# Performance work log

Measured on AMD Instinct MI355X. Metric: run time of the kernel, lower is better.

## Reference

```python
import jax, jax.numpy as jnp
import numpy as np

N = 50000   # nodes
E = 800000  # edges
IN = 128    # input_channels
HID = 256   # hidden_channels
G = 64      # graphs
R = 3       # num_relations
META = 38
EPS = 1e-5


def _glorot(key, shape):
    fan_in, fan_out = shape[-2], shape[-1]
    lim = np.sqrt(6.0 / (fan_in + fan_out)).astype(np.float32)
    return jax.random.uniform(key, shape, jnp.float32, -lim, lim)


def setup_inputs() -> dict:
    key = jax.random.key(0)
    ks = iter(jax.random.split(key, 40))
    inp = {}
    inp["x"] = jax.random.normal(next(ks), (N, IN), jnp.float32)
    inp["edge_attr"] = jax.random.normal(next(ks), (E, 1), jnp.float32)  # unused by module
    inp["edge_index"] = jax.random.randint(next(ks), (2, E), 0, N)
    inp["edge_type"] = jax.random.randint(next(ks), (E,), 0, R)
    inp["MetaData"] = jax.random.normal(next(ks), (G, META), jnp.float32)
    inp["batch"] = jnp.sort(jax.random.randint(next(ks), (N,), 0, G))
    dims = [(IN, 100), (100, HID), (HID, HID), (HID, HID)]
    for l, (din, dout) in enumerate(dims):
        inp[f"W{l}"] = _glorot(next(ks), (R, din, dout))      # per-relation weights
        inp[f"R{l}"] = _glorot(next(ks), (din, dout))          # root weight
        inp[f"b{l}"] = jnp.zeros((dout,), jnp.float32)         # conv bias
        inp[f"g{l}"] = jnp.ones((dout,), jnp.float32)          # BN gamma
        inp[f"bb{l}"] = jnp.zeros((dout,), jnp.float32)        # BN beta
    inp["lin1_w"] = _glorot(next(ks), (HID + META, 100))
    inp["lin1_b"] = jnp.zeros((100,), jnp.float32)
    inp["lin2_w"] = _glorot(next(ks), (100, 1))
    inp["lin2_b"] = jnp.zeros((1,), jnp.float32)
    return inp


def reference(x, edge_attr, edge_index, edge_type, MetaData, batch,
              W0, R0, b0, g0, bb0, W1, R1, b1, g1, bb1,
              W2, R2, b2, g2, bb2, W3, R3, b3, g3, bb3,
              lin1_w, lin1_b, lin2_w, lin2_b):
    src, dst = edge_index[0], edge_index[1]
    seg = edge_type * N + dst  # combined (relation, dst) segment id
    ones_e = jnp.ones((E,), x.dtype)
    cnt = jax.ops.segment_sum(ones_e, seg, num_segments=R * N).reshape(R, N, 1)
    cnt = jnp.maximum(cnt, 1.0)

    def conv(h, W, Rw, b):
        # per-relation transform then gather-scatter mean aggregation (PyG RGCNConv, aggr='mean')
        H = jnp.einsum('ni,rio->rno', h, W)          # [R,N,out]
        msg = H[edge_type, src]                       # [E,out]
        agg = jax.ops.segment_sum(msg, seg, num_segments=R * N)
        agg = agg.reshape(R, N, -1) / cnt
        return agg.sum(0) + h @ Rw + b

    def bn(h, g, bb):  # training-mode BatchNorm1d over nodes
        mu = h.mean(0)
        var = h.var(0)
        return (h - mu) * jax.lax.rsqrt(var + EPS) * g + bb

    for W, Rw, b, g, bb in [(W0, R0, b0, g0, bb0), (W1, R1, b1, g1, bb1),
                            (W2, R2, b2, g2, bb2), (W3, R3, b3, g3, bb3)]:
        x = bn(conv(x, W, Rw, b), g, bb)

    # global_mean_pool
    sums = jax.ops.segment_sum(x, batch, num_segments=G)
    cnts = jax.ops.segment_sum(jnp.ones((N, 1), x.dtype), batch, num_segments=G)
    xg = sums / jnp.maximum(cnts, 1.0)

    h = jnp.concatenate([xg, MetaData], axis=1) @ lin1_w + lin1_b
    # dropout p=0.5 is identity in eval mode
    return h @ lin2_w + lin2_b
```

## Files before the change

### kernel.cpp

```cpp
#include <hip/hip_runtime.h>
#include <hip/hip_bf16.h>

#define NN 50000
#define EE 800000
#define GG 64
#define RR 3
#define METAD 38
#define NSEG (RR*NN)
#define EPSV 1e-5f

typedef __bf16 bf_t;
typedef __attribute__((ext_vector_type(8))) __bf16 bf16x8;
typedef __attribute__((ext_vector_type(4))) __bf16 bf16x4;
typedef __attribute__((ext_vector_type(2))) __bf16 bf16x2;
typedef __attribute__((ext_vector_type(4))) float f32x4;
typedef __attribute__((address_space(1))) void gas_t;
typedef __attribute__((address_space(3))) void las_t;

__device__ __forceinline__ float loadf(const void* p, size_t i, int flag){
  return flag ? ((const float*)p)[i] : (float)(((const bf_t*)p)[i]);
}

__global__ __launch_bounds__(256) void detect_kernel(const void* __restrict__ xraw,
                                                     int* __restrict__ flag){
  __shared__ int found;
  if (threadIdx.x == 0) found = 0;
  __syncthreads();
  const unsigned short* u = (const unsigned short*)xraw;
  for (int i = threadIdx.x; i < 65536; i += 256){
    int e = (u[i] >> 7) & 0xFF;
    if (e >= 0xF0) found = 1;
  }
  __syncthreads();
  if (threadIdx.x == 0) *flag = found;
}

struct CvtJobs {
  const void* src[17];
  float* dst[17];
  int n[17];
};

__global__ __launch_bounds__(256) void cvt_many(CvtJobs j, const int* __restrict__ flag){
  int job = blockIdx.y;
  int i = blockIdx.x*256 + threadIdx.x;
  if (i < j.n[job]) j.dst[job][i] = loadf(j.src[job], i, *flag);
}

__global__ __launch_bounds__(256) void pack_w(const void* __restrict__ W,
                                              const void* __restrict__ R,
                                              bf_t* __restrict__ out,
                                              int D, int O, int dplog,
                                              const int* __restrict__ flag){
  int id = blockIdx.x*256 + threadIdx.x;
  int DP4 = 1 << (dplog + 2);
  int o = id >> (dplog + 2);
  int k = id & (DP4 - 1);
  int r = k >> dplog;
  int i = k & ((1 << dplog) - 1);
  float v = 0.f;
  int fl = *flag;
  if (i < D && o < O){
    if (r < 3) v = loadf(W, ((size_t)r*D + i)*O + o, fl);
    else       v = loadf(R, (size_t)i*O + o, fl);
  }
  out[(size_t)o*DP4 + k] = (bf_t)v;
}

__global__ __launch_bounds__(256) void counti_kernel(const int* __restrict__ ei,
                                                     const int* __restrict__ et,
                                                     int* __restrict__ cnt){
  int e = blockIdx.x*256 + threadIdx.x;
  if (e < EE) atomicAdd(&cnt[et[e]*NN + ei[EE + e]], 1);
}

__global__ __launch_bounds__(256) void rcnt_kernel(const int* __restrict__ cnt,
                                                   float* __restrict__ rcnt){
  int i = blockIdx.x*256 + threadIdx.x;
  if (i < NSEG) rcnt[i] = 1.0f / (float)max(cnt[i], 1);
}

__global__ __launch_bounds__(256) void scan1_kernel(const int* __restrict__ cnt,
                                                    int* __restrict__ segoff,
                                                    int* __restrict__ bsums){
  __shared__ int sh[256];
  int i = blockIdx.x*256 + threadIdx.x;
  int v = (i < NSEG) ? cnt[i] : 0;
  sh[threadIdx.x] = v;
  __syncthreads();
  for (int off = 1; off < 256; off <<= 1){
    int t = 0;
    if (threadIdx.x >= off) t = sh[threadIdx.x - off];
    __syncthreads();
    if (threadIdx.x >= off) sh[threadIdx.x] += t;
    __syncthreads();
  }
  if (i < NSEG) segoff[i] = sh[threadIdx.x] - v;
  if (threadIdx.x == 255) bsums[blockIdx.x] = sh[255];
}

__global__ __launch_bounds__(256) void scan2_kernel(int* __restrict__ bsums, int nb){
  __shared__ int sh[256];
  __shared__ int carry;
  if (threadIdx.x == 0) carry = 0;
  __syncthreads();
  for (int base = 0; base < nb; base += 256){
    int i = base + threadIdx.x;
    int v = (i < nb) ? bsums[i] : 0;
    sh[threadIdx.x] = v;
    __syncthreads();
    for (int off = 1; off < 256; off <<= 1){
      int t = 0;
      if (threadIdx.x >= off) t = sh[threadIdx.x - off];
      __syncthreads();
      if (threadIdx.x >= off) sh[threadIdx.x] += t;
      __syncthreads();
    }
    if (i < nb) bsums[i] = sh[threadIdx.x] - v + carry;
    __syncthreads();
    if (threadIdx.x == 0) carry += sh[255];
    __syncthreads();
  }
}

__global__ __launch_bounds__(256) void scan3_kernel(int* __restrict__ segoff,
                                                    const int* __restrict__ bsums){
  int i = blockIdx.x*256 + threadIdx.x;
  if (i < NSEG) segoff[i] += bsums[blockIdx.x];
  if (i == 0) segoff[NSEG] = EE;
}

__global__ __launch_bounds__(256) void curinit_kernel(const int* __restrict__ segoff,
                                                      int* __restrict__ cursor){
  int i = blockIdx.x*256 + threadIdx.x;
  if (i < NSEG) cursor[i] = segoff[i];
}

__global__ __launch_bounds__(256) void place_kernel(const int* __restrict__ ei,
                                                    const int* __restrict__ et,
                                                    int* __restrict__ cursor,
                                                    int* __restrict__ srcs){
  int e = blockIdx.x*256 + threadIdx.x;
  if (e < EE){
    int seg = et[e]*NN + ei[EE + e];
    int pos = atomicAdd(&cursor[seg], 1);
    srcs[pos] = ei[e];
  }
}

__global__ __launch_bounds__(128) void cvt_x(const void* __restrict__ x,
                                             bf_t* __restrict__ Ab,
                                             const int* __restrict__ flag){
  int d = blockIdx.x, t = threadIdx.x;
  Ab[(size_t)d*512 + 384 + t] = (bf_t)loadf(x, (size_t)d*128 + t, *flag);
}

template<int DP>
__global__ __launch_bounds__(256) void aggregate_wave(const bf_t* __restrict__ Ab, int lda,
                                                      const int* __restrict__ segoff,
                                                      const int* __restrict__ srcs,
                                                      const float* __restrict__ rcnt,
                                                      bf_t* __restrict__ out){
  int wid = (blockIdx.x*256 + threadIdx.x) >> 6;
  if (wid >= NSEG) return;
  int lane = threadIdx.x & 63;
  int r = wid / NN;
  int d = wid - r*NN;
  int s0 = segoff[wid], s1 = segoff[wid + 1];
  const bf_t* in = Ab + 3*DP;

  if (DP == 256){
    float a0=0.f, a1=0.f, a2=0.f, a3=0.f;
    const int off = lane*4;
    int e = s0;
    for (; e + 4 <= s1; e += 4){
      int sA = srcs[e], sB = srcs[e+1], sC = srcs[e+2], sD = srcs[e+3];
      uint2 vA = *(const uint2*)(in + (size_t)sA*lda + off);
      uint2 vB = *(const uint2*)(in + (size_t)sB*lda + off);
      uint2 vC = *(const uint2*)(in + (size_t)sC*lda + off);
      uint2 vD = *(const uint2*)(in + (size_t)sD*lda + off);
      a0 += __uint_as_float(vA.x << 16); a1 += __uint_as_float(vA.x & 0xFFFF0000u);
      a2 += __uint_as_float(vA.y << 16); a3 += __uint_as_float(vA.y & 0xFFFF0000u);
      a0 += __uint_as_float(vB.x << 16); a1 += __uint_as_float(vB.x & 0xFFFF0000u);
      a2 += __uint_as_float(vB.y << 16); a3 += __uint_as_float(vB.y & 0xFFFF0000u);
      a0 += __uint_as_float(vC.x << 16); a1 += __uint_as_float(vC.x & 0xFFFF0000u);
      a2 += __uint_as_float(vC.y << 16); a3 += __uint_as_float(vC.y & 0xFFFF0000u);
      a0 += __uint_as_float(vD.x << 16); a1 += __uint_as_float(vD.x & 0xFFFF0000u);
      a2 += __uint_as_float(vD.y << 16); a3 += __uint_as_float(vD.y & 0xFFFF0000u);
    }
    for (; e < s1; ++e){
      int s = srcs[e];
      uint2 v = *(const uint2*)(in + (size_t)s*lda + off);
      a0 += __uint_as_float(v.x << 16); a1 += __uint_as_float(v.x & 0xFFFF0000u);
      a2 += __uint_as_float(v.y << 16); a3 += __uint_as_float(v.y & 0xFFFF0000u);
    }
    float rc = rcnt[wid];
    bf16x4 o = {(bf_t)(a0*rc), (bf_t)(a1*rc), (bf_t)(a2*rc), (bf_t)(a3*rc)};
    *(bf16x4*)(out + (size_t)d*lda + r*DP + off) = o;
  } else {
    float a0=0.f, a1=0.f;
    const int off = lane*2;
    int e = s0;
    for (; e + 4 <= s1; e += 4){
      int sA = srcs[e], sB = srcs[e+1], sC = srcs[e+2], sD = srcs[e+3];
      unsigned vA = *(const unsigned*)(in + (size_t)sA*lda + off);
      unsigned vB = *(const unsigned*)(in + (size_t)sB*lda + off);
      unsigned vC = *(const unsigned*)(in + (size_t)sC*lda + off);
      unsigned vD = *(const unsigned*)(in + (size_t)sD*lda + off);
      a0 += __uint_as_float(vA << 16); a1 += __uint_as_float(vA & 0xFFFF0000u);
      a0 += __uint_as_float(vB << 16); a1 += __uint_as_float(vB & 0xFFFF0000u);
      a0 += __uint_as_float(vC << 16); a1 += __uint_as_float(vC & 0xFFFF0000u);
      a0 += __uint_as_float(vD << 16); a1 += __uint_as_float(vD & 0xFFFF0000u);
    }
    for (; e < s1; ++e){
      int s = srcs[e];
      unsigned v = *(const unsigned*)(in + (size_t)s*lda + off);
      a0 += __uint_as_float(v << 16); a1 += __uint_as_float(v & 0xFFFF0000u);
    }
    float rc = rcnt[wid];
    bf16x2 o = {(bf_t)(a0*rc), (bf_t)(a1*rc)};
    *(bf16x2*)(out + (size_t)d*lda + r*DP + off) = o;
  }
}

template<int NT>
__global__ __launch_bounds__(512) void gemm_mfma2(const bf_t* __restrict__ A, int lda, int K,
                                                  const bf_t* __restrict__ Bt,
                                                  const float* __restrict__ bias,
                                                  float* __restrict__ C, int ldc, int O,
                                                  float* __restrict__ sums){
  constexpr int NI = NT/64;
  __shared__ uint4 lds4[(128 + NT)*8];
  __shared__ uint4 ldspad[960];
  __shared__ float colsum[2*NT];
  uint4* As4 = lds4;
  uint4* Bs4 = lds4 + 128*8;
  float* stage = (float*)lds4;
  if (K < 0) ((volatile float*)ldspad)[threadIdx.x] = 0.f;

  int tid = threadIdx.x;
  int lane = tid & 63;
  int wave = tid >> 6;
  int row0 = blockIdx.x*128;
  int col0 = blockIdx.y*NT;
  int mw = (wave & 1) << 6;
  int nw = (wave >> 1) * (NT/4);
  int l15 = lane & 15, quad = lane >> 4;
  f32x4 acc[4][NI] = {};

  int lrow = lane >> 3;
  int lk8  = (lane & 7) * 8;
  int ca0 = wave*2, ca1 = wave*2 + 1;
  int gra0 = row0 + ca0*8 + lrow; if (gra0 >= NN) gra0 = NN - 1;
  int gra1 = row0 + ca1*8 + lrow; if (gra1 >= NN) gra1 = NN - 1;
  const bf_t* Ar0 = A + (size_t)gra0*lda + lk8;
  const bf_t* Ar1 = A + (size_t)gra1*lda + lk8;
  const bf_t* Br0 = Bt + (size_t)(col0 + ca0*8 + lrow)*K + lk8;
  const bf_t* Br1 = Bt + (size_t)(col0 + ca1*8 + lrow)*K + lk8;
  uint4* AsD0 = As4 + ca0*64;
  uint4* AsD1 = As4 + ca1*64;
  uint4* BsD0 = Bs4 + ca0*64;
  uint4* BsD1 = Bs4 + ca1*64;

  __builtin_amdgcn_global_load_lds((gas_t*)Ar0, (las_t*)AsD0, 16, 0, 0);
  __builtin_amdgcn_global_load_lds((gas_t*)Ar1, (las_t*)AsD1, 16, 0, 0);
  __builtin_amdgcn_global_load_lds((gas_t*)Br0, (las_t*)BsD0, 16, 0, 0);
  __builtin_amdgcn_global_load_lds((gas_t*)Br1, (las_t*)BsD1, 16, 0, 0);

  int niter = K >> 6;
  for (int i = 0; i < niter; ++i){
    __syncthreads();
    #pragma unroll
    for (int kk = 0; kk < 2; ++kk){
      bf16x8 af[4], bfv[NI];
      int ku = kk*4 + quad;
      #pragma unroll
      for (int mi = 0; mi < 4; ++mi){
        int R = mw + mi*16 + l15;
        af[mi] = *(const bf16x8*)&As4[R*8 + ku];
      }
      #pragma unroll
      for (int ni = 0; ni < NI; ++ni){
        int Rb = nw + ni*16 + l15;
        bfv[ni] = *(const bf16x8*)&Bs4[Rb*8 + ku];
      }
      #pragma unroll
      for (int mi = 0; mi < 4; ++mi)
        #pragma unroll
        for (int ni = 0; ni < NI; ++ni)
          acc[mi][ni] = __builtin_amdgcn_mfma_f32_16x16x32_bf16(af[mi], bfv[ni], acc[mi][ni], 0, 0, 0);
    }
    __syncthreads();
    if (i + 1 < niter){
      int k1 = (i + 1) << 6;
      __builtin_amdgcn_global_load_lds((gas_t*)(Ar0 + k1), (las_t*)AsD0, 16, 0, 0);
      __builtin_amdgcn_global_load_lds((gas_t*)(Ar1 + k1), (las_t*)AsD1, 16, 0, 0);
      __builtin_amdgcn_global_load_lds((gas_t*)(Br0 + k1), (las_t*)BsD0, 16, 0, 0);
      __builtin_amdgcn_global_load_lds((gas_t*)(Br1 + k1), (las_t*)BsD1, 16, 0, 0);
    }
  }

  __syncthreads();
  if (tid < 2*NT) colsum[tid] = 0.f;
  float bzv[NI];
  #pragma unroll
  for (int ni = 0; ni < NI; ++ni){
    int col = col0 + nw + ni*16 + l15;
    bzv[ni] = (col < O) ? bias[col] : 0.f;
  }
  __syncthreads();

  #pragma unroll
  for (int ni = 0; ni < NI; ++ni){
    int lcol = nw + ni*16 + l15;
    int col = col0 + lcol;
    if (col < O){
      float scol = 0.f, qcol = 0.f;
      #pragma unroll
      for (int mi = 0; mi < 4; ++mi){
        int rb = row0 + mw + mi*16 + quad*4;
        #pragma unroll
        for (int j = 0; j < 4; ++j){
          if (rb + j < NN){
            float v = acc[mi][ni][j] + bzv[ni];
            scol += v; qcol += v*v;
          }
        }
      }
      atomicAdd(&colsum[lcol], scol);
      atomicAdd(&colsum[NT + lcol], qcol);
    }
  }

  constexpr int STR = NT + 4;
  constexpr int TPR = NT/4;
  constexpr int RPR = 512/TPR;
  int rl0 = tid / TPR;
  int colg = (tid % TPR)*4;
  #pragma unroll
  for (int c = 0; c < 4; ++c){
    __syncthreads();
    if ((wave & 1) == (c >> 1)){
      int base = (c & 1)*32;
      #pragma unroll
      for (int m2 = 0; m2 < 2; ++m2){
        int mi = (base >> 4) + m2;
        #pragma unroll
        for (int ni = 0; ni < NI; ++ni)
          #pragma unroll
          for (int j = 0; j < 4; ++j)
            stage[(mi*16 + quad*4 + j - base)*STR + nw + ni*16 + l15] = acc[mi][ni][j] + bzv[ni];
      }
    }
    __syncthreads();
    #pragma unroll
    for (int p = 0; p < 32/RPR; ++p){
      int rl = p*RPR + rl0;
      int gr = row0 + c*32 + rl;
      if (gr < NN)
        *(float4*)&C[(size_t)gr*ldc + col0 + colg] = *(const float4*)&stage[rl*STR + colg];
    }
  }

  __syncthreads();
  for (int c = tid; c < NT; c += 512){
    int col = col0 + c;
    if (col < O){
      unsafeAtomicAdd(&sums[col], colsum[c]);
      unsafeAtomicAdd(&sums[256 + col], colsum[NT + c]);
    }
  }
}

__global__ __launch_bounds__(256) void bn_finalize(const float* __restrict__ sums,
                                                   const float* __restrict__ g,
                                                   const float* __restrict__ bb,
                                                   float* __restrict__ scale,
                                                   float* __restrict__ shift, int dout){
  int c = threadIdx.x;
  if (c < dout){
    float mu = sums[c] * (1.0f/NN);
    float var = sums[256 + c] * (1.0f/NN) - mu*mu;
    float rstd = rsqrtf(fmaxf(var, 0.f) + EPSV);
    float s = rstd * g[c];
    scale[c] = s;
    shift[c] = bb[c] - mu*s;
  }
}

template<int DPN>
__global__ __launch_bounds__(DPN) void bn_cvt(const float* __restrict__ C, int ldc, int O,
                                              const float* __restrict__ scale,
                                              const float* __restrict__ shift,
                                              bf_t* __restrict__ Ab, int ldan){
  int d = blockIdx.x, t = threadIdx.x;
  float v = 0.f;
  if (t < O) v = C[(size_t)d*ldc + t]*scale[t] + shift[t];
  Ab[(size_t)d*ldan + 3*DPN + t] = (bf_t)v;
}

__device__ __forceinline__ int lower_bound(const int* __restrict__ a, int v){
  int lo = 0, hi = NN;
  while (lo < hi){ int m = (lo+hi) >> 1; if (a[m] < v) lo = m+1; else hi = m; }
  return lo;
}

__global__ __launch_bounds__(256) void pool_kernel(const bf_t* __restrict__ H,
                                                   const int* __restrict__ batch,
                                                   float* __restrict__ pooled){
  int g = blockIdx.x, sl = blockIdx.y;
  int start = lower_bound(batch, g), end = lower_bound(batch, g+1);
  int len = end - start;
  float inv = 1.0f / (float)max(len, 1);
  int chunk = (len + 7) >> 3;
  int s0 = start + sl*chunk;
  int s1 = min(s0 + chunk, end);
  float s = 0.f;
  for (int n = s0; n < s1; ++n) s += (float)H[(size_t)n*1024 + threadIdx.x];
  if (s1 > s0) unsafeAtomicAdd(&pooled[g*256 + threadIdx.x], s * inv);
}

__global__ __launch_bounds__(128) void final_kernel(const float* __restrict__ pooled,
                                                    const float* __restrict__ meta,
                                                    const float* __restrict__ w1,
                                                    const float* __restrict__ b1,
                                                    const float* __restrict__ w2,
                                                    const float* __restrict__ b2,
                                                    void* __restrict__ out,
                                                    const int* __restrict__ flag){
  int g = blockIdx.x;
  __shared__ float h1[100];
  __shared__ float red[128];
  int t = threadIdx.x;
  if (t < 100){
    float acc = b1[t];
    for (int k = 0; k < 256; ++k) acc += pooled[g*256 + k] * w1[k*100 + t];
    for (int k = 0; k < METAD; ++k) acc += meta[g*METAD + k] * w1[(256+k)*100 + t];
    h1[t] = acc;
  }
  __syncthreads();
  red[t] = (t < 100) ? h1[t] * w2[t] : 0.f;
  __syncthreads();
  for (int s = 64; s > 0; s >>= 1){
    if (t < s) red[t] += red[t + s];
    __syncthreads();
  }
  if (t == 0){
    float v = red[0] + b2[0];
    if (*flag) ((float*)out)[g] = v;
    else       ((__hip_bfloat16*)out)[g] = __float2bfloat16(v);
  }
}

extern "C" void kernel_launch(void* const* d_in, const int* in_sizes, int n_in,
                              void* d_out, int out_size, void* d_ws, size_t ws_size,
                              hipStream_t stream){
  const void* x    = d_in[0];
  const int*  ei   = (const int*)d_in[2];
  const int*  et   = (const int*)d_in[3];
  const int*  batch= (const int*)d_in[5];

  float* ws     = (float*)d_ws;
  int*   flag   = (int*)ws;
  float* rcnt   = ws + 16;
  int*   cnt    = (int*)(ws + 150016);
  int*   segoff = (int*)(ws + 300032);
  int*   bsums  = (int*)(ws + 450048);
  int*   srcs   = (int*)(ws + 451072);
  float* sums   = ws + 1251072;
  float* scale  = ws + 1251584;
  float* shift  = ws + 1251840;
  float* pooled = ws + 1252096;
  float* bc     = ws + 1268480;
  float* gc_    = ws + 1269348;
  float* bbc    = ws + 1270216;
  float* metaf  = ws + 1271084;
  float* w1f    = ws + 1273516;
  float* b1f    = ws + 1302916;
  float* w2f    = ws + 1303016;
  float* b2f_   = ws + 1303116;
  bf_t*  wt     = (bf_t*)(ws + 1303168);
  int*   cursor = (int*)(ws + 1663616);
  float* C      = ws + 1813632;
  bf_t*  Ab     = (bf_t*)(ws + 14613632);

  const size_t wtoff[4] = {0, 65536, 196608, 458752};

  detect_kernel<<<1, 256, 0, stream>>>(x, flag);

  const int vsz[4]  = {100, 256, 256, 256};
  const int voff[4] = {0, 100, 356, 612};
  float *bfp[4], *gf[4], *bbf[4];
  CvtJobs J;
  int nj = 0;
  for (int l = 0; l < 4; ++l){
    bfp[l] = bc + voff[l]; gf[l] = gc_ + voff[l]; bbf[l] = bbc + voff[l];
    J.src[nj] = d_in[6 + l*5 + 2]; J.dst[nj] = bfp[l]; J.n[nj] = vsz[l]; nj++;
    J.src[nj] = d_in[6 + l*5 + 3]; J.dst[nj] = gf[l];  J.n[nj] = vsz[l]; nj++;
    J.src[nj] = d_in[6 + l*5 + 4]; J.dst[nj] = bbf[l]; J.n[nj] = vsz[l]; nj++;
  }
  J.src[nj] = d_in[4];  J.dst[nj] = metaf; J.n[nj] = GG*METAD; nj++;
  J.src[nj] = d_in[26]; J.dst[nj] = w1f;   J.n[nj] = 29400; nj++;
  J.src[nj] = d_in[27]; J.dst[nj] = b1f;   J.n[nj] = 100; nj++;
  J.src[nj] = d_in[28]; J.dst[nj] = w2f;   J.n[nj] = 100; nj++;
  J.src[nj] = d_in[29]; J.dst[nj] = b2f_;  J.n[nj] = 1; nj++;
  cvt_many<<<dim3(115, nj), 256, 0, stream>>>(J, flag);

  const int din[4] = {128, 100, 256, 256};
  const int dou[4] = {100, 256, 256, 256};
  const int DP[4]  = {128, 128, 256, 256};
  const int dplog[4] = {7, 7, 8, 8};
  const int Op[4]  = {128, 256, 256, 256};
  for (int l = 0; l < 4; ++l){
    int total = Op[l] << (dplog[l] + 2);
    pack_w<<<total/256, 256, 0, stream>>>(d_in[6 + l*5 + 0], d_in[6 + l*5 + 1],
                                          wt + wtoff[l], din[l], dou[l], dplog[l], flag);
  }

  hipMemsetAsync(cnt, 0, NSEG*sizeof(int), stream);
  counti_kernel<<<(EE+255)/256, 256, 0, stream>>>(ei, et, cnt);
  rcnt_kernel<<<(NSEG+255)/256, 256, 0, stream>>>(cnt, rcnt);
  int nb = (NSEG + 255)/256;
  scan1_kernel<<<nb, 256, 0, stream>>>(cnt, segoff, bsums);
  scan2_kernel<<<1, 256, 0, stream>>>(bsums, nb);
  scan3_kernel<<<nb, 256, 0, stream>>>(segoff, bsums);
  curinit_kernel<<<nb, 256, 0, stream>>>(segoff, cursor);
  place_kernel<<<(EE+255)/256, 256, 0, stream>>>(ei, et, cursor, srcs);

  cvt_x<<<NN, 128, 0, stream>>>(x, Ab, flag);

  const int lda[4] = {512, 512, 1024, 1024};
  int aggBlocks = (NSEG + 3)/4;
  for (int l = 0; l < 4; ++l){
    int O = dou[l];
    if (DP[l] == 128)
      aggregate_wave<128><<<aggBlocks, 256, 0, stream>>>(Ab, lda[l], segoff, srcs, rcnt, Ab);
    else
      aggregate_wave<256><<<aggBlocks, 256, 0, stream>>>(Ab, lda[l], segoff, srcs, rcnt, Ab);

    hipMemsetAsync(sums, 0, 512*sizeof(float), stream);
    dim3 g2(391, Op[l]/128);
    gemm_mfma2<128><<<g2, 512, 0, stream>>>(Ab, lda[l], 4*DP[l], wt + wtoff[l], bfp[l],
                                            C, Op[l], O, sums);

    bn_finalize<<<1, 256, 0, stream>>>(sums, gf[l], bbf[l], scale, shift, O);

    int DPN = (l < 3) ? DP[l+1] : 256;
    int ldan = (l < 3) ? lda[l+1] : 1024;
    if (DPN == 128)
      bn_cvt<128><<<NN, 128, 0, stream>>>(C, Op[l], O, scale, shift, Ab, ldan);
    else
      bn_cvt<256><<<NN, 256, 0, stream>>>(C, Op[l], O, scale, shift, Ab, ldan);
  }

  hipMemsetAsync(pooled, 0, (size_t)GG*256*sizeof(float), stream);
  pool_kernel<<<dim3(GG, 8), 256, 0, stream>>>(Ab + 768, batch, pooled);
  final_kernel<<<GG, 128, 0, stream>>>(pooled, metaf, w1f, b1f, w2f, b2f_, d_out, flag);
}
```

Before: 938.2 us.

## Double-buffer GEMM LDS tiles and XOR-swizzle K chunks to avoid bank conflicts

The MFMA GEMM now keeps two LDS stages and prefetches the tile two iterations ahead with async global-to-LDS loads. It waits with explicit vmcnt counts instead of a full sync before each compute step. The K-chunk index is XOR-swizzled by row on both the load and the read side to cut LDS bank conflicts, and the old padding array used to tune occupancy is dropped. The extra LDS per block may lower occupancy, and the hand-written waitcnt/barrier sequence relies on the compiler keeping the expected number of in-flight loads.

New measurement: 872.2 us. 7.0% less time.

```diff
diff --git a/kernel.cpp b/kernel.cpp
--- a/kernel.cpp
+++ b/kernel.cpp
@@ -223,6 +223,13 @@
   }
 }
 
+#define ISSUE4(B_, KO_)                                                                             \
+  { uint4* _b = &lds4[B_][0];                                                                       \
+    __builtin_amdgcn_global_load_lds((gas_t*)(Ar0 + (KO_)), (las_t*)(_b + ca0*64), 16, 0, 0);       \
+    __builtin_amdgcn_global_load_lds((gas_t*)(Ar1 + (KO_)), (las_t*)(_b + ca1*64), 16, 0, 0);       \
+    __builtin_amdgcn_global_load_lds((gas_t*)(Br0 + (KO_)), (las_t*)(_b + 128*8 + ca0*64), 16, 0, 0); \
+    __builtin_amdgcn_global_load_lds((gas_t*)(Br1 + (KO_)), (las_t*)(_b + 128*8 + ca1*64), 16, 0, 0); }
+
 template<int NT>
 __global__ __launch_bounds__(512) void gemm_mfma2(const bf_t* __restrict__ A, int lda, int K,
                                                   const bf_t* __restrict__ Bt,
@@ -230,13 +237,9 @@
                                                   float* __restrict__ C, int ldc, int O,
                                                   float* __restrict__ sums){
   constexpr int NI = NT/64;
-  __shared__ uint4 lds4[(128 + NT)*8];
-  __shared__ uint4 ldspad[960];
+  __shared__ uint4 lds4[2][(128 + NT)*8];
   __shared__ float colsum[2*NT];
-  uint4* As4 = lds4;
-  uint4* Bs4 = lds4 + 128*8;
   float* stage = (float*)lds4;
-  if (K < 0) ((volatile float*)ldspad)[threadIdx.x] = 0.f;
 
   int tid = threadIdx.x;
   int lane = tid & 63;
@@ -249,7 +252,7 @@
   f32x4 acc[4][NI] = {};
 
   int lrow = lane >> 3;
-  int lk8  = (lane & 7) * 8;
+  int lk8  = ((lane & 7) ^ lrow) * 8;
   int ca0 = wave*2, ca1 = wave*2 + 1;
   int gra0 = row0 + ca0*8 + lrow; if (gra0 >= NN) gra0 = NN - 1;
   int gra1 = row0 + ca1*8 + lrow; if (gra1 >= NN) gra1 = NN - 1;
@@ -257,32 +260,34 @@
   const bf_t* Ar1 = A + (size_t)gra1*lda + lk8;
   const bf_t* Br0 = Bt + (size_t)(col0 + ca0*8 + lrow)*K + lk8;
   const bf_t* Br1 = Bt + (size_t)(col0 + ca1*8 + lrow)*K + lk8;
-  uint4* AsD0 = As4 + ca0*64;
-  uint4* AsD1 = As4 + ca1*64;
-  uint4* BsD0 = Bs4 + ca0*64;
-  uint4* BsD1 = Bs4 + ca1*64;
-
-  __builtin_amdgcn_global_load_lds((gas_t*)Ar0, (las_t*)AsD0, 16, 0, 0);
-  __builtin_amdgcn_global_load_lds((gas_t*)Ar1, (las_t*)AsD1, 16, 0, 0);
-  __builtin_amdgcn_global_load_lds((gas_t*)Br0, (las_t*)BsD0, 16, 0, 0);
-  __builtin_amdgcn_global_load_lds((gas_t*)Br1, (las_t*)BsD1, 16, 0, 0);
 
   int niter = K >> 6;
+  ISSUE4(0, 0)
+  if (niter > 1) ISSUE4(1, 64)
+
   for (int i = 0; i < niter; ++i){
-    __syncthreads();
+    if (i + 1 < niter) asm volatile("s_waitcnt vmcnt(4)" ::: "memory");
+    else               asm volatile("s_waitcnt vmcnt(0)" ::: "memory");
+    __builtin_amdgcn_s_barrier();
+    asm volatile("" ::: "memory");
+    __builtin_amdgcn_sched_barrier(0);
+
+    const uint4* As4 = &lds4[i & 1][0];
+    const uint4* Bs4 = As4 + 128*8;
     #pragma unroll
     for (int kk = 0; kk < 2; ++kk){
       bf16x8 af[4], bfv[NI];
       int ku = kk*4 + quad;
+      int kswz = ku ^ (l15 & 7);
       #pragma unroll
       for (int mi = 0; mi < 4; ++mi){
         int R = mw + mi*16 + l15;
-        af[mi] = *(const bf16x8*)&As4[R*8 + ku];
+        af[mi] = *(const bf16x8*)&As4[R*8 + kswz];
       }
       #pragma unroll
       for (int ni = 0; ni < NI; ++ni){
         int Rb = nw + ni*16 + l15;
-        bfv[ni] = *(const bf16x8*)&Bs4[Rb*8 + ku];
+        bfv[ni] = *(const bf16x8*)&Bs4[Rb*8 + kswz];
       }
       #pragma unroll
       for (int mi = 0; mi < 4; ++mi)
@@ -290,14 +295,9 @@
         for (int ni = 0; ni < NI; ++ni)
           acc[mi][ni] = __builtin_amdgcn_mfma_f32_16x16x32_bf16(af[mi], bfv[ni], acc[mi][ni], 0, 0, 0);
     }
-    __syncthreads();
-    if (i + 1 < niter){
-      int k1 = (i + 1) << 6;
-      __builtin_amdgcn_global_load_lds((gas_t*)(Ar0 + k1), (las_t*)AsD0, 16, 0, 0);
-      __builtin_amdgcn_global_load_lds((gas_t*)(Ar1 + k1), (las_t*)AsD1, 16, 0, 0);
-      __builtin_amdgcn_global_load_lds((gas_t*)(Br0 + k1), (las_t*)BsD0, 16, 0, 0);
-      __builtin_amdgcn_global_load_lds((gas_t*)(Br1 + k1), (las_t*)BsD1, 16, 0, 0);
-    }
+    asm volatile("s_waitcnt lgkmcnt(0)" ::: "memory");
+    __builtin_amdgcn_s_barrier();
+    if (i + 2 < niter) ISSUE4(i & 1, (i + 2) << 6)
   }
 
   __syncthreads();
```
